# Optimization experiments

Measured on AMD Instinct MI355X. Metric: run time of the kernel, lower is better.

Reference implementation:

```python
import math
import jax, jax.numpy as jnp
import numpy as np

B, S, IN_DIM = 8, 1024, 3
D, H, FF, L, OUT = 512, 8, 2048, 4, 6
DH = D // H


def layernorm(x, g, b, eps=1e-5):
    mu = jnp.mean(x, axis=-1, keepdims=True)
    var = jnp.mean((x - mu) ** 2, axis=-1, keepdims=True)
    return (x - mu) * jax.lax.rsqrt(var + eps) * g + b


def positional_encoding(seq_len, d):
    pos = jnp.arange(seq_len, dtype=jnp.float32)[:, None]
    div = jnp.exp(jnp.arange(0, d, 2, dtype=jnp.float32) * (-math.log(10000.0) / d))
    pe = jnp.zeros((seq_len, d), dtype=jnp.float32)
    pe = pe.at[:, 0::2].set(jnp.sin(pos * div))
    pe = pe.at[:, 1::2].set(jnp.cos(pos * div))
    return pe  # [S, D]


def setup_inputs() -> dict:
    key = jax.random.key(0)
    ks = jax.random.split(key, 16)
    s = 0.02
    inp = {
        'x': jax.random.normal(ks[0], (B, S, IN_DIM), dtype=jnp.float32),
        'Wproj': jax.random.normal(ks[1], (IN_DIM, D), dtype=jnp.float32) * s,
        'bproj': jnp.zeros((D,), jnp.float32),
        'gp': jnp.ones((D,), jnp.float32), 'bp': jnp.zeros((D,), jnp.float32),
        'Wq': jax.random.normal(ks[2], (L, D, D), dtype=jnp.float32) * s,
        'Wk': jax.random.normal(ks[3], (L, D, D), dtype=jnp.float32) * s,
        'Wv': jax.random.normal(ks[4], (L, D, D), dtype=jnp.float32) * s,
        'Wo': jax.random.normal(ks[5], (L, D, D), dtype=jnp.float32) * s,
        'g1': jnp.ones((L, D), jnp.float32), 'b1': jnp.zeros((L, D), jnp.float32),
        'W1': jax.random.normal(ks[6], (L, D, FF), dtype=jnp.float32) * s,
        'W2': jax.random.normal(ks[7], (L, FF, D), dtype=jnp.float32) * s,
        'g2': jnp.ones((L, D), jnp.float32), 'b2': jnp.zeros((L, D), jnp.float32),
        'gf': jnp.ones((D,), jnp.float32), 'bf': jnp.zeros((D,), jnp.float32),
        'Wout': jax.random.normal(ks[8], (D, OUT), dtype=jnp.float32) * s,
        'bout': jnp.zeros((OUT,), jnp.float32),
    }
    return inp


def reference(x, Wproj, bproj, gp, bp, Wq, Wk, Wv, Wo, g1, b1,
              W1, W2, g2, b2, gf, bf, Wout, bout):
    # padding mask: True where all features are zero
    mask = jnp.sum(jnp.abs(x), axis=-1) == 0  # [B, S]
    h = x @ Wproj + bproj                     # [B, S, D]
    h = h + positional_encoding(h.shape[1], D)[None]
    h = layernorm(h, gp, bp)
    scale = 1.0 / math.sqrt(DH)
    for l in range(L):
        q = (h @ Wq[l]).reshape(B, S, H, DH)
        k = (h @ Wk[l]).reshape(B, S, H, DH)
        v = (h @ Wv[l]).reshape(B, S, H, DH)
        scores = jnp.einsum('bqhd,bkhd->bhqk', q, k) * scale  # [B,H,S,S]
        scores = jnp.where(mask[:, None, None, :], -jnp.inf, scores)
        attn = jax.nn.softmax(scores, axis=-1)
        o = jnp.einsum('bhqk,bkhd->bqhd', attn, v).reshape(B, S, D) @ Wo[l]
        h = layernorm(h + o, g1[l], b1[l])
        ff = jax.nn.silu(h @ W1[l]) @ W2[l]
        h = layernorm(h + ff, g2[l], b2[l])
    h = layernorm(h, gf, bf)
    not_pad = (~mask).astype(h.dtype)                      # [B, S]
    pooled = jnp.sum(h * not_pad[..., None], axis=1) / (
        jnp.sum(not_pad, axis=1, keepdims=True) + 1e-8)    # [B, D]
    return pooled @ Wout + bout                            # [B, OUT]
```

## Files before the change

### kernel.cpp

```cpp
#include <hip/hip_runtime.h>
#include <math.h>
#include <stdint.h>

namespace {

constexpr int Bc = 8, Sc = 1024, Dc = 512, Hc = 8, FFc = 2048, Lc = 4, OUTc = 6;
constexpr int QS = 1536;

typedef __attribute__((ext_vector_type(8))) short  bf16x8;
typedef __attribute__((ext_vector_type(4))) float  f32x4;

__device__ __forceinline__ void ld4(float d[4], const float* s) {
    float4 t = *(const float4*)s;
    d[0] = t.x; d[1] = t.y; d[2] = t.z; d[3] = t.w;
}
__device__ __forceinline__ float bf2f_s(short u) {
    union { uint32_t i; float f; } c; c.i = ((uint32_t)(unsigned short)u) << 16; return c.f;
}
__device__ __forceinline__ unsigned short f2bf(float f) {
    union { float f; uint32_t i; } c; c.f = f;
    uint32_t r = c.i + 0x7FFF + ((c.i >> 16) & 1);
    return (unsigned short)(r >> 16);
}
__device__ __forceinline__ unsigned short f2bf_fast(float f) {
    union { float f; uint32_t i; } c; c.f = f;
    return (unsigned short)((c.i + 0x8000u) >> 16);
}

#define GLDS16(gp, lp) __builtin_amdgcn_global_load_lds(                      \
    (const __attribute__((address_space(1))) uint32_t*)(gp),                  \
    (__attribute__((address_space(3))) uint32_t*)(lp), 16, 0, 0)

__global__ __launch_bounds__(256) void castAll(
    const float* __restrict__ Wq, const float* __restrict__ Wk,
    const float* __restrict__ Wv, const float* __restrict__ Wo,
    const float* __restrict__ W1, const float* __restrict__ W2,
    unsigned short* __restrict__ qkvT, unsigned short* __restrict__ WoT,
    unsigned short* __restrict__ W1T, unsigned short* __restrict__ W2T)
{
    const int t = blockIdx.x;
    const float* in; unsigned short* out; int K, N, k0, n0;
    if (t < 1024) {
        const int mat = t >> 6, l = mat >> 2, w = mat & 3;
        K = 512; N = 512;
        k0 = ((t >> 3) & 7) << 6; n0 = (t & 7) << 6;
        const float* ws4[4] = {Wq, Wk, Wv, Wo};
        in = ws4[w] + (size_t)l * 512 * 512;
        out = (w < 3) ? qkvT + (size_t)l * QS * 512 + (size_t)w * 512 * 512
                      : WoT + (size_t)l * 512 * 512;
    } else if (t < 2048) {
        const int u = t - 1024, l = u >> 8;
        K = 512; N = 2048;
        k0 = ((u >> 5) & 7) << 6; n0 = (u & 31) << 6;
        in = W1 + (size_t)l * 512 * 2048;
        out = W1T + (size_t)l * 2048 * 512;
    } else {
        const int u = t - 2048, l = u >> 8;
        K = 2048; N = 512;
        k0 = ((u >> 3) & 31) << 6; n0 = (u & 7) << 6;
        in = W2 + (size_t)l * 2048 * 512;
        out = W2T + (size_t)l * 512 * 2048;
    }
    __shared__ float tbuf[64][65];
    const int c = threadIdx.x & 63, r4 = threadIdx.x >> 6;
    #pragma unroll
    for (int it = 0; it < 16; ++it) {
        const int r = (it << 2) + r4;
        tbuf[r][c] = in[(size_t)(k0 + r) * N + n0 + c];
    }
    __syncthreads();
    #pragma unroll
    for (int it = 0; it < 16; ++it) {
        const int r = (it << 2) + r4;
        out[(size_t)(n0 + r) * K + k0 + c] = f2bf(tbuf[c][r]);
    }
}

__global__ __launch_bounds__(256) void proj_pe_ln(
    const float* __restrict__ x, const float* __restrict__ Wproj,
    const float* __restrict__ bproj, const float* __restrict__ gp,
    const float* __restrict__ bp, unsigned short* __restrict__ hbf,
    float* __restrict__ notpad, float* __restrict__ maskadd)
{
    const int wave = threadIdx.x >> 6, lane = threadIdx.x & 63;
    const int tok = (blockIdx.x << 2) + wave;
    const int s = tok & (Sc - 1);
    const float x0 = x[tok * 3 + 0], x1 = x[tok * 3 + 1], x2 = x[tok * 3 + 2];
    if (lane == 0) {
        const bool pad = (fabsf(x0) + fabsf(x1) + fabsf(x2) == 0.0f);
        notpad[tok]  = pad ? 0.0f : 1.0f;
        maskadd[tok] = pad ? -1e30f : 0.0f;
    }
    const float c = -logf(10000.0f) / (float)Dc;
    float v[8];
    float sum = 0.f, sumsq = 0.f;
    const int d0 = lane << 3;
    #pragma unroll
    for (int j = 0; j < 8; ++j) {
        const int d = d0 + j;
        float val = fmaf(x0, Wproj[d],
                    fmaf(x1, Wproj[Dc + d],
                    fmaf(x2, Wproj[2 * Dc + d], bproj[d])));
        const float arg = (float)s * expf((float)(d & ~1) * c);
        val += (d & 1) ? cosf(arg) : sinf(arg);
        v[j] = val;
        sum += val; sumsq += val * val;
    }
    #pragma unroll
    for (int m = 1; m < 64; m <<= 1) {
        sum   += __shfl_xor(sum, m, 64);
        sumsq += __shfl_xor(sumsq, m, 64);
    }
    const float mu = sum * (1.0f / Dc);
    const float rstd = rsqrtf(sumsq * (1.0f / Dc) - mu * mu + 1e-5f);
    float gg[8], bb[8];
    ld4(gg, gp + d0); ld4(gg + 4, gp + d0 + 4);
    ld4(bb, bp + d0); ld4(bb + 4, bp + d0 + 4);
    bf16x8 rb;
    #pragma unroll
    for (int j = 0; j < 8; ++j)
        rb[j] = (short)f2bf((v[j] - mu) * rstd * gg[j] + bb[j]);
    *(bf16x8*)(hbf + (size_t)tok * Dc + d0) = rb;
}

__global__ __launch_bounds__(256) void add_ln(
    const unsigned short* __restrict__ hin, const unsigned short* __restrict__ delta,
    const float* __restrict__ g, const float* __restrict__ b,
    unsigned short* __restrict__ hout)
{
    const int wave = threadIdx.x >> 6, lane = threadIdx.x & 63;
    const int tok = (blockIdx.x << 2) + wave;
    const int d0 = lane << 3;
    const size_t base = (size_t)tok * Dc + d0;
    const bf16x8 hv = *(const bf16x8*)(hin + base);
    const bf16x8 dv = *(const bf16x8*)(delta + base);
    float v[8];
    float sum = 0.f, sumsq = 0.f;
    #pragma unroll
    for (int j = 0; j < 8; ++j) {
        v[j] = bf2f_s(hv[j]) + bf2f_s(dv[j]);
        sum += v[j]; sumsq += v[j] * v[j];
    }
    #pragma unroll
    for (int m = 1; m < 64; m <<= 1) {
        sum   += __shfl_xor(sum, m, 64);
        sumsq += __shfl_xor(sumsq, m, 64);
    }
    const float mu = sum * (1.0f / Dc);
    const float rstd = rsqrtf(sumsq * (1.0f / Dc) - mu * mu + 1e-5f);
    float gg[8], bb[8];
    ld4(gg, g + d0); ld4(gg + 4, g + d0 + 4);
    ld4(bb, b + d0); ld4(bb + 4, b + d0 + 4);
    bf16x8 rb;
    #pragma unroll
    for (int j = 0; j < 8; ++j)
        rb[j] = (short)f2bf((v[j] - mu) * rstd * gg[j] + bb[j]);
    *(bf16x8*)(hout + base) = rb;
}

template<int EPI, int NT>
__global__ __launch_bounds__(256) void gemm_bf16(
    const unsigned short* __restrict__ A, const unsigned short* __restrict__ Bt,
    void* __restrict__ Cv, void* __restrict__ Cv2, int M, int N, int K)
{
    constexpr int JN = NT / 32;
    constexpr int TR = 140;
    constexpr int ABsz = 128 * 64 + NT * 64;
    constexpr int SMsz = (EPI == 3 && 128 * TR > ABsz) ? 128 * TR : ABsz;
    __shared__ unsigned short smem[SMsz];
    unsigned short* As = smem;
    unsigned short* Bs = smem + 128 * 64;
    const int tid = threadIdx.x;
    const int wave = tid >> 6, lane = tid & 63;
    const int m0 = blockIdx.y << 7;
    const int n0 = blockIdx.x * NT;
    const int wm = (wave >> 1) << 6;
    const int wn = (wave & 1) * (NT / 2);
    const int l15 = lane & 15;
    const int lg  = lane >> 4;
    const int grow  = lane >> 3;
    const int gcolk = ((lane & 7) ^ grow) << 3;

    f32x4 acc[4][JN] = {};

    for (int k0 = 0; k0 < K; k0 += 64) {
        __syncthreads();
        #pragma unroll
        for (int t = 0; t < 4; ++t) {
            const int rb = (t << 5) + (wave << 3);
            GLDS16(A + (size_t)(m0 + rb + grow) * K + k0 + gcolk, &As[rb * 64]);
        }
        #pragma unroll
        for (int t = 0; t < NT / 32; ++t) {
            const int rb = (t << 5) + (wave << 3);
            GLDS16(Bt + (size_t)(n0 + rb + grow) * K + k0 + gcolk, &Bs[rb * 64]);
        }
        __syncthreads();
        #pragma unroll
        for (int h = 0; h < 2; ++h) {
            const int sw = (((h << 2) + lg) ^ (l15 & 7)) << 3;
            bf16x8 af[4], bfr[JN];
            #pragma unroll
            for (int i = 0; i < 4; ++i)
                af[i] = *(const bf16x8*)&As[(wm + (i << 4) + l15) * 64 + sw];
            #pragma unroll
            for (int j = 0; j < JN; ++j)
                bfr[j] = *(const bf16x8*)&Bs[(wn + (j << 4) + l15) * 64 + sw];
            #pragma unroll
            for (int i = 0; i < 4; ++i)
                #pragma unroll
                for (int j = 0; j < JN; ++j)
                    acc[i][j] = __builtin_amdgcn_mfma_f32_16x16x32_bf16(
                        af[i], bfr[j], acc[i][j], 0, 0, 0);
        }
    }

    if constexpr (EPI == 3) {
        if (n0 >= 1024) {
            __syncthreads();
            unsigned short* Tr = smem;
            #pragma unroll
            for (int i = 0; i < 4; ++i)
                #pragma unroll
                for (int j = 0; j < JN; ++j)
                    #pragma unroll
                    for (int r = 0; r < 4; ++r)
                        Tr[(wn + (j << 4) + l15) * TR + wm + (i << 4) + (lg << 2) + r]
                            = f2bf(acc[i][j][r]);
            __syncthreads();
            const int bb = m0 >> 10, s0 = m0 & 1023;
            #pragma unroll
            for (int it = 0; it < 8; ++it) {
                const int idx = (it << 8) + tid;
                const int ln = idx >> 4, lmc = (idx & 15) << 3;
                const int gcol = n0 - 1024 + ln;
                const int head = gcol >> 6, dh = gcol & 63;
                *(bf16x8*)((unsigned short*)Cv2 +
                    (size_t)((((bb << 3) + head) << 6) + dh) * 1024 + s0 + lmc) =
                    *(const bf16x8*)&Tr[ln * TR + lmc];
            }
            return;
        }
    }

    const float qsc = 0.125f * 1.44269504f;
    const int crow0 = m0 + wm + (lg << 2);
    const int ccol0 = n0 + wn + l15;
    #pragma unroll
    for (int i = 0; i < 4; ++i)
        #pragma unroll
        for (int j = 0; j < JN; ++j)
            #pragma unroll
            for (int r = 0; r < 4; ++r) {
                const int row = crow0 + (i << 4) + r;
                const int col = ccol0 + (j << 4);
                float v = acc[i][j][r];
                if (EPI == 3) {
                    if (n0 < 512) v *= qsc;
                    ((unsigned short*)Cv)[(size_t)row * 1024 + col] = f2bf(v);
                } else {
                    if (EPI == 1) v = v / (1.0f + expf(-v));
                    ((unsigned short*)Cv)[(size_t)row * N + col] = f2bf(v);
                }
            }
}

__global__ __launch_bounds__(256) void attn_mfma(
    const unsigned short* __restrict__ qk,
    const unsigned short* __restrict__ vT,
    const float* __restrict__ maskadd,
    unsigned short* __restrict__ o)
{
    constexpr int PST = 132;
    __shared__ unsigned short Ks[2][128][32];
    __shared__ unsigned short Vs[4][64][32];
    __shared__ unsigned short Ps[4][16][PST];
    __shared__ float Madd[128];
    const int tid = threadIdx.x;
    const int wave = tid >> 6, lane = tid & 63;
    const int b  = blockIdx.x & 7;
    const int hh = (blockIdx.x >> 3) & 7;
    const int qt = blockIdx.x >> 6;
    const int q0 = qt << 7;
    const int l15 = lane & 15, lg = lane >> 4;
    const int srow = lane >> 2;
    const int scol = (lane & 3) << 3;

    #pragma unroll
    for (int t = 0; t < 2; ++t)
        #pragma unroll
        for (int p = 0; p < 2; ++p)
            GLDS16(qk + (size_t)((b << 10) + q0 + (t << 6) + (wave << 4) + srow) * 1024
                      + (hh << 6) + (p << 5) + scol,
                   &Ks[p][(t << 6) + (wave << 4)][0]);
    __syncthreads();
    bf16x8 qf[2][2];
    #pragma unroll
    for (int s = 0; s < 2; ++s)
        #pragma unroll
        for (int p = 0; p < 2; ++p)
            qf[s][p] = *(const bf16x8*)&Ks[p][(s << 6) + (wave << 4) + l15][lg << 3];

    f32x4 oacc[2][4] = {};
    float l_part[2][4] = {};

    for (int kt = 0; kt < 8; ++kt) {
        const int k0 = kt << 7;
        __syncthreads();
        #pragma unroll
        for (int t = 0; t < 2; ++t)
            #pragma unroll
            for (int p = 0; p < 2; ++p)
                GLDS16(qk + (size_t)((b << 10) + k0 + (t << 6) + (wave << 4) + srow) * 1024
                          + 512 + (hh << 6) + (p << 5) + scol,
                       &Ks[p][(t << 6) + (wave << 4)][0]);
        #pragma unroll
        for (int kp = 0; kp < 4; ++kp)
            GLDS16(vT + (size_t)((((b << 3) + hh) << 6) + (wave << 4) + srow) * 1024
                      + k0 + (kp << 5) + scol,
                   &Vs[kp][wave << 4][0]);
        if (tid < 128) Madd[tid] = maskadd[(b << 10) + k0 + tid];
        __syncthreads();

        f32x4 sacc[2][8] = {};
        #pragma unroll
        for (int j = 0; j < 8; ++j) {
            const bf16x8 kf0 = *(const bf16x8*)&Ks[0][(j << 4) + l15][lg << 3];
            const bf16x8 kf1 = *(const bf16x8*)&Ks[1][(j << 4) + l15][lg << 3];
            #pragma unroll
            for (int s = 0; s < 2; ++s) {
                sacc[s][j] = __builtin_amdgcn_mfma_f32_16x16x32_bf16(qf[s][0], kf0, sacc[s][j], 0, 0, 0);
                sacc[s][j] = __builtin_amdgcn_mfma_f32_16x16x32_bf16(qf[s][1], kf1, sacc[s][j], 0, 0, 0);
            }
        }

        bf16x8 vf[4][4];
        #pragma unroll
        for (int kp = 0; kp < 4; ++kp)
            #pragma unroll
            for (int j = 0; j < 4; ++j)
                vf[kp][j] = *(const bf16x8*)&Vs[kp][(j << 4) + l15][lg << 3];

        float ma[8];
        #pragma unroll
        for (int j = 0; j < 8; ++j) ma[j] = Madd[(j << 4) + l15];

        #pragma unroll
        for (int s = 0; s < 2; ++s) {
            #pragma unroll
            for (int j = 0; j < 8; ++j)
                #pragma unroll
                for (int r = 0; r < 4; ++r) {
                    const float p = exp2f(sacc[s][j][r] + ma[j]);
                    l_part[s][r] += p;
                    Ps[wave][(lg << 2) + r][(j << 4) + l15] = f2bf_fast(p);
                }
            __asm__ volatile("s_waitcnt lgkmcnt(0)" ::: "memory");
            #pragma unroll
            for (int kp = 0; kp < 4; ++kp) {
                const bf16x8 pa = *(const bf16x8*)&Ps[wave][l15][(kp << 5) + (lg << 3)];
                #pragma unroll
                for (int j = 0; j < 4; ++j)
                    oacc[s][j] = __builtin_amdgcn_mfma_f32_16x16x32_bf16(pa, vf[kp][j], oacc[s][j], 0, 0, 0);
            }
            __asm__ volatile("s_waitcnt lgkmcnt(0)" ::: "memory");
        }
    }

    #pragma unroll
    for (int s = 0; s < 2; ++s)
        #pragma unroll
        for (int r = 0; r < 4; ++r) {
            float l = l_part[s][r];
            #pragma unroll
            for (int m = 1; m < 16; m <<= 1) l += __shfl_xor(l, m, 64);
            l_part[s][r] = 1.0f / l;
        }
    #pragma unroll
    for (int s = 0; s < 2; ++s) {
        const int tokr = (b << 10) + q0 + (s << 6) + (wave << 4) + (lg << 2);
        #pragma unroll
        for (int j = 0; j < 4; ++j)
            #pragma unroll
            for (int r = 0; r < 4; ++r)
                o[(size_t)(tokr + r) * 512 + (hh << 6) + (j << 4) + l15] =
                    f2bf(oacc[s][j][r] * l_part[s][r]);
    }
}

__global__ __launch_bounds__(256) void pool_ln(
    const unsigned short* __restrict__ hbf, const float* __restrict__ notpad,
    const float* __restrict__ gf, const float* __restrict__ bfp,
    float* __restrict__ pooled, float* __restrict__ counts)
{
    __shared__ float sh[512];
    const int b = blockIdx.y, s0 = blockIdx.x << 5;
    const int wave = threadIdx.x >> 6, lane = threadIdx.x & 63;
    const int d0 = lane << 3;
    float gg[8], bb[8];
    ld4(gg, gf + d0); ld4(gg + 4, gf + d0 + 4);
    ld4(bb, bfp + d0); ld4(bb + 4, bfp + d0 + 4);
    float accv[8] = {};
    for (int t = 0; t < 8; ++t) {
        const int tok = (b << 10) + s0 + (wave << 3) + t;
        const float w = notpad[tok];
        const bf16x8 hv = *(const bf16x8*)(hbf + (size_t)tok * Dc + d0);
        float v[8], sum = 0.f, sumsq = 0.f;
        #pragma unroll
        for (int j = 0; j < 8; ++j) {
            v[j] = bf2f_s(hv[j]); sum += v[j]; sumsq += v[j] * v[j];
        }
        #pragma unroll
        for (int m = 1; m < 64; m <<= 1) {
            sum   += __shfl_xor(sum, m, 64);
            sumsq += __shfl_xor(sumsq, m, 64);
        }
        const float mu = sum * (1.0f / Dc);
        const float rstd = rsqrtf(sumsq * (1.0f / Dc) - mu * mu + 1e-5f);
        #pragma unroll
        for (int j = 0; j < 8; ++j)
            accv[j] = fmaf(w, (v[j] - mu) * rstd * gg[j] + bb[j], accv[j]);
    }
    sh[threadIdx.x] = 0.f; sh[threadIdx.x + 256] = 0.f;
    __syncthreads();
    #pragma unroll
    for (int j = 0; j < 8; ++j) atomicAdd(&sh[d0 + j], accv[j]);
    __syncthreads();
    atomicAdd(&pooled[b * Dc + threadIdx.x], sh[threadIdx.x]);
    atomicAdd(&pooled[b * Dc + 256 + threadIdx.x], sh[threadIdx.x + 256]);
    if (threadIdx.x < 32) {
        float w = notpad[(b << 10) + s0 + threadIdx.x];
        #pragma unroll
        for (int m = 1; m < 32; m <<= 1) w += __shfl_xor(w, m, 64);
        if (threadIdx.x == 0) atomicAdd(&counts[b], w);
    }
}

__global__ void out_kernel(
    const float* __restrict__ pooled, const float* __restrict__ counts,
    const float* __restrict__ Wout, const float* __restrict__ bout,
    float* __restrict__ out)
{
    const int bo = blockIdx.x;
    const int b = bo / OUTc, oc = bo % OUTc;
    const int lane = threadIdx.x;
    float acc = 0.f;
    for (int d = lane; d < Dc; d += 64)
        acc = fmaf(pooled[b * Dc + d], Wout[(size_t)d * OUTc + oc], acc);
    #pragma unroll
    for (int m = 1; m < 64; m <<= 1) acc += __shfl_xor(acc, m, 64);
    if (lane == 0) out[b * OUTc + oc] = acc / (counts[b] + 1e-8f) + bout[oc];
}

}

extern "C" void kernel_launch(void* const* d_in, const int* in_sizes, int n_in,
                              void* d_out, int out_size, void* d_ws, size_t ws_size,
                              hipStream_t stream)
{
    (void)in_sizes; (void)n_in; (void)out_size; (void)ws_size;
    const float* x     = (const float*)d_in[0];
    const float* Wproj = (const float*)d_in[1];
    const float* bproj = (const float*)d_in[2];
    const float* gp    = (const float*)d_in[3];
    const float* bp    = (const float*)d_in[4];
    const float* Wq    = (const float*)d_in[5];
    const float* Wk    = (const float*)d_in[6];
    const float* Wv    = (const float*)d_in[7];
    const float* Wo    = (const float*)d_in[8];
    const float* g1    = (const float*)d_in[9];
    const float* b1    = (const float*)d_in[10];
    const float* W1    = (const float*)d_in[11];
    const float* W2    = (const float*)d_in[12];
    const float* g2    = (const float*)d_in[13];
    const float* b2    = (const float*)d_in[14];
    const float* gf    = (const float*)d_in[15];
    const float* bf    = (const float*)d_in[16];
    const float* Wout  = (const float*)d_in[17];
    const float* bout  = (const float*)d_in[18];
    float* out = (float*)d_out;

    const size_t MiB = 1u << 20;
    char* base = (char*)d_ws;
    unsigned short* h_bf    = (unsigned short*)(base);
    unsigned short* qk_act  = (unsigned short*)(base + 24 * MiB);
    unsigned short* vT      = (unsigned short*)(base + 40 * MiB);
    unsigned short* ob_bf   = (unsigned short*)(base + 48 * MiB);
    unsigned short* bufB_bf = (unsigned short*)(base + 56 * MiB);
    unsigned short* ffa_bf  = (unsigned short*)(base + 24 * MiB);
    unsigned short* qkvT    = (unsigned short*)(base + 72 * MiB);
    unsigned short* WoT     = (unsigned short*)(base + 78 * MiB);
    unsigned short* W1T     = (unsigned short*)(base + 80 * MiB);
    unsigned short* W2T     = (unsigned short*)(base + 88 * MiB);
    float*          notpad  = (float*)(base + 96 * MiB);
    float*          maskadd = notpad + 8192;
    float*          pooled  = maskadd + 8192;
    float*          counts  = pooled + Bc * Dc;

    const int M = Bc * Sc;

    castAll<<<3072, 256, 0, stream>>>(Wq, Wk, Wv, Wo, W1, W2, qkvT, WoT, W1T, W2T);
    proj_pe_ln<<<M / 4, 256, 0, stream>>>(x, Wproj, bproj, gp, bp, h_bf, notpad, maskadd);

    for (int l = 0; l < Lc; ++l) {
        gemm_bf16<3, 128><<<dim3(QS / 128, M / 128), 256, 0, stream>>>(
            h_bf, qkvT + (size_t)l * QS * 512, qk_act, vT, M, QS, 512);
        attn_mfma<<<Bc * Hc * (Sc / 128), 256, 0, stream>>>(qk_act, vT, maskadd, ob_bf);
        gemm_bf16<2, 64><<<dim3(512 / 64, M / 128), 256, 0, stream>>>(
            ob_bf, WoT + (size_t)l * 512 * 512, bufB_bf, nullptr, M, 512, 512);
        add_ln<<<M / 4, 256, 0, stream>>>(h_bf, bufB_bf, g1 + (size_t)l * Dc, b1 + (size_t)l * Dc, h_bf);
        gemm_bf16<1, 128><<<dim3(FFc / 128, M / 128), 256, 0, stream>>>(
            h_bf, W1T + (size_t)l * FFc * 512, ffa_bf, nullptr, M, FFc, 512);
        gemm_bf16<2, 64><<<dim3(512 / 64, M / 128), 256, 0, stream>>>(
            ffa_bf, W2T + (size_t)l * 512 * FFc, bufB_bf, nullptr, M, 512, FFc);
        add_ln<<<M / 4, 256, 0, stream>>>(h_bf, bufB_bf, g2 + (size_t)l * Dc, b2 + (size_t)l * Dc, h_bf);
    }

    hipMemsetAsync(pooled, 0, (size_t)(Bc * Dc + Bc) * sizeof(float), stream);
    pool_ln<<<dim3(Sc / 32, Bc), 256, 0, stream>>>(h_bf, notpad, gf, bf, pooled, counts);
    out_kernel<<<Bc * OUTc, 64, 0, stream>>>(pooled, counts, Wout, bout, out);
}
```

Baseline: 824.1 us.

## Fold LayerNorm into GEMMs via weight folding and epilogue partial stats

Removes the standalone add+LayerNorm kernels. Gamma and beta are folded into the QKV and W1 weights at cast time, along with correction vectors, so the following GEMM epilogue applies the normalization from per-row mean and rstd. The Wo and W2 GEMM epilogues now do the residual add on the un-normalized stream and write per-row partial sum and sum-of-squares, which the next kernel reduces. This saves two full activation read/write passes per layer, at the cost of heavier epilogues, atomics in the weight cast, and different bf16 rounding points.

```diff
diff --git a/kernel.cpp b/kernel.cpp
--- a/kernel.cpp
+++ b/kernel.cpp
@@ -13,6 +13,9 @@
 __device__ __forceinline__ void ld4(float d[4], const float* s) {
     float4 t = *(const float4*)s;
     d[0] = t.x; d[1] = t.y; d[2] = t.z; d[3] = t.w;
+}
+__device__ __forceinline__ float bf2f_u(unsigned short u) {
+    union { uint32_t i; float f; } c; c.i = ((uint32_t)u) << 16; return c.f;
 }
 __device__ __forceinline__ float bf2f_s(short u) {
     union { uint32_t i; float f; } c; c.i = ((uint32_t)(unsigned short)u) << 16; return c.f;
@@ -35,25 +38,44 @@
     const float* __restrict__ Wq, const float* __restrict__ Wk,
     const float* __restrict__ Wv, const float* __restrict__ Wo,
     const float* __restrict__ W1, const float* __restrict__ W2,
+    const float* __restrict__ gp, const float* __restrict__ bp,
+    const float* __restrict__ g1, const float* __restrict__ b1,
+    const float* __restrict__ g2, const float* __restrict__ b2,
     unsigned short* __restrict__ qkvT, unsigned short* __restrict__ WoT,
-    unsigned short* __restrict__ W1T, unsigned short* __restrict__ W2T)
+    unsigned short* __restrict__ W1T, unsigned short* __restrict__ W2T,
+    float* __restrict__ c1qkv, float* __restrict__ c2qkv,
+    float* __restrict__ c1w1, float* __restrict__ c2w1)
 {
     const int t = blockIdx.x;
     const float* in; unsigned short* out; int K, N, k0, n0;
+    bool fold = false;
+    const float *gamma = nullptr, *beta = nullptr;
+    float *cv1 = nullptr, *cv2 = nullptr;
     if (t < 1024) {
         const int mat = t >> 6, l = mat >> 2, w = mat & 3;
         K = 512; N = 512;
         k0 = ((t >> 3) & 7) << 6; n0 = (t & 7) << 6;
         const float* ws4[4] = {Wq, Wk, Wv, Wo};
         in = ws4[w] + (size_t)l * 512 * 512;
-        out = (w < 3) ? qkvT + (size_t)l * QS * 512 + (size_t)w * 512 * 512
-                      : WoT + (size_t)l * 512 * 512;
+        if (w < 3) {
+            out = qkvT + (size_t)l * QS * 512 + (size_t)w * 512 * 512;
+            fold = true;
+            gamma = (l == 0) ? gp : g2 + (size_t)(l - 1) * 512;
+            beta  = (l == 0) ? bp : b2 + (size_t)(l - 1) * 512;
+            cv1 = c1qkv + (size_t)l * QS + w * 512;
+            cv2 = c2qkv + (size_t)l * QS + w * 512;
+        } else {
+            out = WoT + (size_t)l * 512 * 512;
+        }
     } else if (t < 2048) {
         const int u = t - 1024, l = u >> 8;
         K = 512; N = 2048;
         k0 = ((u >> 5) & 7) << 6; n0 = (u & 31) << 6;
         in = W1 + (size_t)l * 512 * 2048;
         out = W1T + (size_t)l * 2048 * 512;
+        fold = true;
+        gamma = g1 + (size_t)l * 512; beta = b1 + (size_t)l * 512;
+        cv1 = c1w1 + (size_t)l * 2048; cv2 = c2w1 + (size_t)l * 2048;
     } else {
         const int u = t - 2048, l = u >> 8;
         K = 2048; N = 512;
@@ -62,7 +84,12 @@
         out = W2T + (size_t)l * 512 * 2048;
     }
     __shared__ float tbuf[64][65];
+    __shared__ float gls[64], bls[64];
     const int c = threadIdx.x & 63, r4 = threadIdx.x >> 6;
+    if (fold && threadIdx.x < 64) {
+        gls[threadIdx.x] = gamma[k0 + threadIdx.x];
+        bls[threadIdx.x] = beta[k0 + threadIdx.x];
+    }
     #pragma unroll
     for (int it = 0; it < 16; ++it) {
         const int r = (it << 2) + r4;
@@ -72,15 +99,28 @@
     #pragma unroll
     for (int it = 0; it < 16; ++it) {
         const int r = (it << 2) + r4;
-        out[(size_t)(n0 + r) * K + k0 + c] = f2bf(tbuf[c][r]);
-    }
-}
-
-__global__ __launch_bounds__(256) void proj_pe_ln(
+        float v = tbuf[c][r];
+        if (fold) v *= gls[c];
+        out[(size_t)(n0 + r) * K + k0 + c] = f2bf(v);
+    }
+    if (fold && threadIdx.x < 64) {
+        float a1 = 0.f, a2 = 0.f;
+        #pragma unroll
+        for (int cc = 0; cc < 64; ++cc) {
+            const float w = tbuf[cc][threadIdx.x];
+            a1 = fmaf(gls[cc], w, a1);
+            a2 = fmaf(bls[cc], w, a2);
+        }
+        atomicAdd(cv1 + n0 + threadIdx.x, a1);
+        atomicAdd(cv2 + n0 + threadIdx.x, a2);
+    }
+}
+
+__global__ __launch_bounds__(256) void proj_pe(
     const float* __restrict__ x, const float* __restrict__ Wproj,
-    const float* __restrict__ bproj, const float* __restrict__ gp,
-    const float* __restrict__ bp, unsigned short* __restrict__ hbf,
-    float* __restrict__ notpad, float* __restrict__ maskadd)
+    const float* __restrict__ bproj, unsigned short* __restrict__ res,
+    float* __restrict__ stats, float* __restrict__ notpad,
+    float* __restrict__ maskadd)
 {
     const int wave = threadIdx.x >> 6, lane = threadIdx.x & 63;
     const int tok = (blockIdx.x << 2) + wave;
@@ -92,9 +132,9 @@
         maskadd[tok] = pad ? -1e30f : 0.0f;
     }
     const float c = -logf(10000.0f) / (float)Dc;
-    float v[8];
+    const int d0 = lane << 3;
     float sum = 0.f, sumsq = 0.f;
-    const int d0 = lane << 3;
+    bf16x8 rb;
     #pragma unroll
     for (int j = 0; j < 8; ++j) {
         const int d = d0 + j;
@@ -103,71 +143,38 @@
                     fmaf(x2, Wproj[2 * Dc + d], bproj[d])));
         const float arg = (float)s * expf((float)(d & ~1) * c);
         val += (d & 1) ? cosf(arg) : sinf(arg);
-        v[j] = val;
-        sum += val; sumsq += val * val;
-    }
+        rb[j] = (short)f2bf(val);
+        const float rv = bf2f_s(rb[j]);
+        sum += rv; sumsq += rv * rv;
+    }
+    *(bf16x8*)(res + (size_t)tok * Dc + d0) = rb;
     #pragma unroll
     for (int m = 1; m < 64; m <<= 1) {
         sum   += __shfl_xor(sum, m, 64);
         sumsq += __shfl_xor(sumsq, m, 64);
     }
-    const float mu = sum * (1.0f / Dc);
-    const float rstd = rsqrtf(sumsq * (1.0f / Dc) - mu * mu + 1e-5f);
-    float gg[8], bb[8];
-    ld4(gg, gp + d0); ld4(gg + 4, gp + d0 + 4);
-    ld4(bb, bp + d0); ld4(bb + 4, bp + d0 + 4);
-    bf16x8 rb;
-    #pragma unroll
-    for (int j = 0; j < 8; ++j)
-        rb[j] = (short)f2bf((v[j] - mu) * rstd * gg[j] + bb[j]);
-    *(bf16x8*)(hbf + (size_t)tok * Dc + d0) = rb;
-}
-
-__global__ __launch_bounds__(256) void add_ln(
-    const unsigned short* __restrict__ hin, const unsigned short* __restrict__ delta,
-    const float* __restrict__ g, const float* __restrict__ b,
-    unsigned short* __restrict__ hout)
-{
-    const int wave = threadIdx.x >> 6, lane = threadIdx.x & 63;
-    const int tok = (blockIdx.x << 2) + wave;
-    const int d0 = lane << 3;
-    const size_t base = (size_t)tok * Dc + d0;
-    const bf16x8 hv = *(const bf16x8*)(hin + base);
-    const bf16x8 dv = *(const bf16x8*)(delta + base);
-    float v[8];
-    float sum = 0.f, sumsq = 0.f;
-    #pragma unroll
-    for (int j = 0; j < 8; ++j) {
-        v[j] = bf2f_s(hv[j]) + bf2f_s(dv[j]);
-        sum += v[j]; sumsq += v[j] * v[j];
-    }
-    #pragma unroll
-    for (int m = 1; m < 64; m <<= 1) {
-        sum   += __shfl_xor(sum, m, 64);
-        sumsq += __shfl_xor(sumsq, m, 64);
-    }
-    const float mu = sum * (1.0f / Dc);
-    const float rstd = rsqrtf(sumsq * (1.0f / Dc) - mu * mu + 1e-5f);
-    float gg[8], bb[8];
-    ld4(gg, g + d0); ld4(gg + 4, g + d0 + 4);
-    ld4(bb, b + d0); ld4(bb + 4, b + d0 + 4);
-    bf16x8 rb;
-    #pragma unroll
-    for (int j = 0; j < 8; ++j)
-        rb[j] = (short)f2bf((v[j] - mu) * rstd * gg[j] + bb[j]);
-    *(bf16x8*)(hout + base) = rb;
+    if (lane == 0) {
+        stats[(size_t)tok * 32 + 0] = sum;
+        stats[(size_t)tok * 32 + 1] = sumsq;
+    }
 }
 
 template<int EPI, int NT>
 __global__ __launch_bounds__(256) void gemm_bf16(
     const unsigned short* __restrict__ A, const unsigned short* __restrict__ Bt,
-    void* __restrict__ Cv, void* __restrict__ Cv2, int M, int N, int K)
+    void* __restrict__ Cv, void* __restrict__ Cv2,
+    const float* __restrict__ statsIn, int npart,
+    const float* __restrict__ c1, const float* __restrict__ c2,
+    const unsigned short* __restrict__ resIn,
+    const float* __restrict__ gcol, const float* __restrict__ bcol,
+    float* __restrict__ partOut, int M, int N, int K)
 {
     constexpr int JN = NT / 32;
     constexpr int TR = 140;
     constexpr int ABsz = 128 * 64 + NT * 64;
     constexpr int SMsz = (EPI == 3 && 128 * TR > ABsz) ? 128 * TR : ABsz;
     __shared__ unsigned short smem[SMsz];
+    __shared__ float muS[128], rsS[128];
     unsigned short* As = smem;
     unsigned short* Bs = smem + 128 * 64;
     const int tid = threadIdx.x;
@@ -215,61 +222,114 @@
         }
     }
 
-    if constexpr (EPI == 3) {
-        if (n0 >= 1024) {
-            __syncthreads();
-            unsigned short* Tr = smem;
-            #pragma unroll
-            for (int i = 0; i < 4; ++i)
-                #pragma unroll
-                for (int j = 0; j < JN; ++j)
+    __syncthreads();
+    if (tid < 128) {
+        float s1 = 0.f, s2 = 0.f;
+        const float* pr = statsIn + (size_t)(m0 + tid) * 32;
+        for (int p = 0; p < npart; ++p) { s1 += pr[2 * p]; s2 += pr[2 * p + 1]; }
+        const float mu = s1 * (1.0f / 512.0f);
+        muS[tid] = mu;
+        rsS[tid] = rsqrtf(s2 * (1.0f / 512.0f) - mu * mu + 1e-5f);
+    }
+    __syncthreads();
+
+    if constexpr (EPI == 3 || EPI == 1) {
+        float c1v[JN], c2v[JN];
+        const int ccol0 = n0 + wn + l15;
+        #pragma unroll
+        for (int j = 0; j < JN; ++j) {
+            c1v[j] = c1[ccol0 + (j << 4)];
+            c2v[j] = c2[ccol0 + (j << 4)];
+        }
+        if constexpr (EPI == 3) {
+            if (n0 >= 1024) {
+                unsigned short* Tr = smem;
+                #pragma unroll
+                for (int i = 0; i < 4; ++i)
                     #pragma unroll
-                    for (int r = 0; r < 4; ++r)
-                        Tr[(wn + (j << 4) + l15) * TR + wm + (i << 4) + (lg << 2) + r]
-                            = f2bf(acc[i][j][r]);
-            __syncthreads();
-            const int bb = m0 >> 10, s0 = m0 & 1023;
-            #pragma unroll
-            for (int it = 0; it < 8; ++it) {
-                const int idx = (it << 8) + tid;
-                const int ln = idx >> 4, lmc = (idx & 15) << 3;
-                const int gcol = n0 - 1024 + ln;
-                const int head = gcol >> 6, dh = gcol & 63;
-                *(bf16x8*)((unsigned short*)Cv2 +
-                    (size_t)((((bb << 3) + head) << 6) + dh) * 1024 + s0 + lmc) =
-                    *(const bf16x8*)&Tr[ln * TR + lmc];
+                    for (int j = 0; j < JN; ++j)
+                        #pragma unroll
+                        for (int r = 0; r < 4; ++r) {
+                            const int lr = wm + (i << 4) + (lg << 2) + r;
+                            const float v = rsS[lr] * (acc[i][j][r] - muS[lr] * c1v[j]) + c2v[j];
+                            Tr[(wn + (j << 4) + l15) * TR + lr] = f2bf(v);
+                        }
+                __syncthreads();
+                const int bb = m0 >> 10, s0 = m0 & 1023;
+                #pragma unroll
+                for (int it = 0; it < 8; ++it) {
+                    const int idx = (it << 8) + tid;
+                    const int ln = idx >> 4, lmc = (idx & 15) << 3;
+                    const int gcol2 = n0 - 1024 + ln;
+                    const int head = gcol2 >> 6, dh = gcol2 & 63;
+                    *(bf16x8*)((unsigned short*)Cv2 +
+                        (size_t)((((bb << 3) + head) << 6) + dh) * 1024 + s0 + lmc) =
+                        *(const bf16x8*)&smem[ln * TR + lmc];
+                }
+                return;
             }
-            return;
-        }
-    }
-
-    const float qsc = 0.125f * 1.44269504f;
-    const int crow0 = m0 + wm + (lg << 2);
-    const int ccol0 = n0 + wn + l15;
-    #pragma unroll
-    for (int i = 0; i < 4; ++i)
-        #pragma unroll
-        for (int j = 0; j < JN; ++j)
+        }
+        const float qsc = 0.125f * 1.44269504f;
+        #pragma unroll
+        for (int i = 0; i < 4; ++i)
+            #pragma unroll
+            for (int j = 0; j < JN; ++j)
+                #pragma unroll
+                for (int r = 0; r < 4; ++r) {
+                    const int lr = wm + (i << 4) + (lg << 2) + r;
+                    const int row = m0 + lr;
+                    const int col = ccol0 + (j << 4);
+                    float v = rsS[lr] * (acc[i][j][r] - muS[lr] * c1v[j]) + c2v[j];
+                    if (EPI == 3) {
+                        if (n0 < 512) v *= qsc;
+                        ((unsigned short*)Cv)[(size_t)row * 1024 + col] = f2bf(v);
+                    } else {
+                        v = v / (1.0f + expf(-v));
+                        ((unsigned short*)Cv)[(size_t)row * N + col] = f2bf(v);
+                    }
+                }
+    } else {
+        float gv[JN], bv[JN];
+        const int ccol0 = n0 + wn + l15;
+        #pragma unroll
+        for (int j = 0; j < JN; ++j) {
+            gv[j] = gcol[ccol0 + (j << 4)];
+            bv[j] = bcol[ccol0 + (j << 4)];
+        }
+        const int slot = (blockIdx.x << 1) | (wave & 1);
+        #pragma unroll
+        for (int i = 0; i < 4; ++i)
             #pragma unroll
             for (int r = 0; r < 4; ++r) {
-                const int row = crow0 + (i << 4) + r;
-                const int col = ccol0 + (j << 4);
-                float v = acc[i][j][r];
-                if (EPI == 3) {
-                    if (n0 < 512) v *= qsc;
-                    ((unsigned short*)Cv)[(size_t)row * 1024 + col] = f2bf(v);
-                } else {
-                    if (EPI == 1) v = v / (1.0f + expf(-v));
-                    ((unsigned short*)Cv)[(size_t)row * N + col] = f2bf(v);
+                const int lr = wm + (i << 4) + (lg << 2) + r;
+                const int row = m0 + lr;
+                float s1 = 0.f, s2 = 0.f;
+                #pragma unroll
+                for (int j = 0; j < JN; ++j) {
+                    const int col = ccol0 + (j << 4);
+                    const float hp = bf2f_u(resIn[(size_t)row * 512 + col]);
+                    const float hn = (hp - muS[lr]) * rsS[lr] * gv[j] + bv[j];
+                    const unsigned short rb = f2bf(hn + acc[i][j][r]);
+                    ((unsigned short*)Cv)[(size_t)row * 512 + col] = rb;
+                    const float rv = bf2f_u(rb);
+                    s1 += rv; s2 += rv * rv;
+                }
+                #pragma unroll
+                for (int m = 1; m < 16; m <<= 1) {
+                    s1 += __shfl_xor(s1, m, 64);
+                    s2 += __shfl_xor(s2, m, 64);
+                }
+                if (l15 == 0) {
+                    partOut[(size_t)row * 32 + slot * 2 + 0] = s1;
+                    partOut[(size_t)row * 32 + slot * 2 + 1] = s2;
                 }
             }
+    }
 }
 
 __global__ __launch_bounds__(256) void attn_mfma(
-    const unsigned short* __restrict__ qk,
-    const unsigned short* __restrict__ vT,
-    const float* __restrict__ maskadd,
-    unsigned short* __restrict__ o)
+    const unsigned short* __restrict__ qk, const unsigned short* __restrict__ vT,
+    const float* __restrict__ maskadd, unsigned short* __restrict__ o)
 {
     constexpr int PST = 132;
     __shared__ unsigned short Ks[2][128][32];
@@ -389,7 +449,9 @@
 }
 
 __global__ __launch_bounds__(256) void pool_ln(
-    const unsigned short* __restrict__ hbf, const float* __restrict__ notpad,
+    const unsigned short* __restrict__ res, const float* __restrict__ stats,
+    const float* __restrict__ notpad,
+    const float* __restrict__ g2l, const float* __restrict__ b2l,
     const float* __restrict__ gf, const float* __restrict__ bfp,
     float* __restrict__ pooled, float* __restrict__ counts)
 {
@@ -397,18 +459,30 @@
     const int b = blockIdx.y, s0 = blockIdx.x << 5;
     const int wave = threadIdx.x >> 6, lane = threadIdx.x & 63;
     const int d0 = lane << 3;
-    float gg[8], bb[8];
+    float g2v[8], b2v[8], gg[8], bb[8];
+    ld4(g2v, g2l + d0); ld4(g2v + 4, g2l + d0 + 4);
+    ld4(b2v, b2l + d0); ld4(b2v + 4, b2l + d0 + 4);
     ld4(gg, gf + d0); ld4(gg + 4, gf + d0 + 4);
     ld4(bb, bfp + d0); ld4(bb + 4, bfp + d0 + 4);
     float accv[8] = {};
     for (int t = 0; t < 8; ++t) {
         const int tok = (b << 10) + s0 + (wave << 3) + t;
         const float w = notpad[tok];
-        const bf16x8 hv = *(const bf16x8*)(hbf + (size_t)tok * Dc + d0);
-        float v[8], sum = 0.f, sumsq = 0.f;
+        float s1 = stats[(size_t)tok * 32 + ((lane & 15) << 1)];
+        float s2 = stats[(size_t)tok * 32 + ((lane & 15) << 1) + 1];
+        #pragma unroll
+        for (int m = 1; m < 16; m <<= 1) {
+            s1 += __shfl_xor(s1, m, 64);
+            s2 += __shfl_xor(s2, m, 64);
+        }
+        const float mu2 = s1 * (1.0f / Dc);
+        const float rs2 = rsqrtf(s2 * (1.0f / Dc) - mu2 * mu2 + 1e-5f);
+        const bf16x8 hv = *(const bf16x8*)(res + (size_t)tok * Dc + d0);
+        float h2[8], sum = 0.f, sumsq = 0.f;
         #pragma unroll
         for (int j = 0; j < 8; ++j) {
-            v[j] = bf2f_s(hv[j]); sum += v[j]; sumsq += v[j] * v[j];
+            h2[j] = (bf2f_s(hv[j]) - mu2) * rs2 * g2v[j] + b2v[j];
+            sum += h2[j]; sumsq += h2[j] * h2[j];
         }
         #pragma unroll
         for (int m = 1; m < 64; m <<= 1) {
@@ -419,7 +493,7 @@
         const float rstd = rsqrtf(sumsq * (1.0f / Dc) - mu * mu + 1e-5f);
         #pragma unroll
         for (int j = 0; j < 8; ++j)
-            accv[j] = fmaf(w, (v[j] - mu) * rstd * gg[j] + bb[j], accv[j]);
+            accv[j] = fmaf(w, (h2[j] - mu) * rstd * gg[j] + bb[j], accv[j]);
     }
     sh[threadIdx.x] = 0.f; sh[threadIdx.x + 256] = 0.f;
     __syncthreads();
@@ -482,41 +556,59 @@
 
     const size_t MiB = 1u << 20;
     char* base = (char*)d_ws;
-    unsigned short* h_bf    = (unsigned short*)(base);
+    unsigned short* res     = (unsigned short*)(base);
+    unsigned short* res1    = (unsigned short*)(base + 8 * MiB);
+    float*          partA   = (float*)(base + 16 * MiB);
+    float*          partB   = (float*)(base + 17 * MiB);
+    float*          cvec    = (float*)(base + 18 * MiB);
+    float*          c1qkv   = cvec;
+    float*          c2qkv   = cvec + 6144;
+    float*          c1w1    = cvec + 12288;
+    float*          c2w1    = cvec + 20480;
+    float*          pooled  = cvec + 28672;
+    float*          counts  = cvec + 32768;
+    float*          notpad  = (float*)(base + 19 * MiB);
+    float*          maskadd = notpad + 8192;
     unsigned short* qk_act  = (unsigned short*)(base + 24 * MiB);
     unsigned short* vT      = (unsigned short*)(base + 40 * MiB);
     unsigned short* ob_bf   = (unsigned short*)(base + 48 * MiB);
-    unsigned short* bufB_bf = (unsigned short*)(base + 56 * MiB);
     unsigned short* ffa_bf  = (unsigned short*)(base + 24 * MiB);
     unsigned short* qkvT    = (unsigned short*)(base + 72 * MiB);
     unsigned short* WoT     = (unsigned short*)(base + 78 * MiB);
     unsigned short* W1T     = (unsigned short*)(base + 80 * MiB);
     unsigned short* W2T     = (unsigned short*)(base + 88 * MiB);
-    float*          notpad  = (float*)(base + 96 * MiB);
-    float*          maskadd = notpad + 8192;
-    float*          pooled  = maskadd + 8192;
-    float*          counts  = pooled + Bc * Dc;
 
     const int M = Bc * Sc;
 
-    castAll<<<3072, 256, 0, stream>>>(Wq, Wk, Wv, Wo, W1, W2, qkvT, WoT, W1T, W2T);
-    proj_pe_ln<<<M / 4, 256, 0, stream>>>(x, Wproj, bproj, gp, bp, h_bf, notpad, maskadd);
+    hipMemsetAsync(cvec, 0, (size_t)(32768 + 8) * sizeof(float), stream);
+    castAll<<<3072, 256, 0, stream>>>(Wq, Wk, Wv, Wo, W1, W2,
+        gp, bp, g1, b1, g2, b2, qkvT, WoT, W1T, W2T, c1qkv, c2qkv, c1w1, c2w1);
+    proj_pe<<<M / 4, 256, 0, stream>>>(x, Wproj, bproj, res, partA, notpad, maskadd);
 
     for (int l = 0; l < Lc; ++l) {
+        const int np = (l == 0) ? 1 : 16;
+        const float* gprev = (l == 0) ? gp : g2 + (size_t)(l - 1) * 512;
+        const float* bprev = (l == 0) ? bp : b2 + (size_t)(l - 1) * 512;
         gemm_bf16<3, 128><<<dim3(QS / 128, M / 128), 256, 0, stream>>>(
-            h_bf, qkvT + (size_t)l * QS * 512, qk_act, vT, M, QS, 512);
+            res, qkvT + (size_t)l * QS * 512, qk_act, vT,
+            partA, np, c1qkv + (size_t)l * QS, c2qkv + (size_t)l * QS,
+            nullptr, nullptr, nullptr, nullptr, M, QS, 512);
         attn_mfma<<<Bc * Hc * (Sc / 128), 256, 0, stream>>>(qk_act, vT, maskadd, ob_bf);
-        gemm_bf16<2, 64><<<dim3(512 / 64, M / 128), 256, 0, stream>>>(
-            ob_bf, WoT + (size_t)l * 512 * 512, bufB_bf, nullptr, M, 512, 512);
-        add_ln<<<M / 4, 256, 0, stream>>>(h_bf, bufB_bf, g1 + (size_t)l * Dc, b1 + (size_t)l * Dc, h_bf);
+        gemm_bf16<4, 64><<<dim3(512 / 64, M / 128), 256, 0, stream>>>(
+            ob_bf, WoT + (size_t)l * 512 * 512, res1, nullptr,
+            partA, np, nullptr, nullptr, res, gprev, bprev, partB, M, 512, 512);
         gemm_bf16<1, 128><<<dim3(FFc / 128, M / 128), 256, 0, stream>>>(
-            h_bf, W1T + (size_t)l * FFc * 512, ffa_bf, nullptr, M, FFc, 512);
-        gemm_bf16<2, 64><<<dim3(512 / 64, M / 128), 256, 0, stream>>>(
-            ffa_bf, W2T + (size_t)l * 512 * FFc, bufB_bf, nullptr, M, 512, FFc);
-        add_ln<<<M / 4, 256, 0, stream>>>(h_bf, bufB_bf, g2 + (size_t)l * Dc, b2 + (size_t)l * Dc, h_bf);
-    }
-
-    hipMemsetAsync(pooled, 0, (size_t)(Bc * Dc + Bc) * sizeof(float), stream);
-    pool_ln<<<dim3(Sc / 32, Bc), 256, 0, stream>>>(h_bf, notpad, gf, bf, pooled, counts);
+            res1, W1T + (size_t)l * FFc * 512, ffa_bf, nullptr,
+            partB, 16, c1w1 + (size_t)l * FFc, c2w1 + (size_t)l * FFc,
+            nullptr, nullptr, nullptr, nullptr, M, FFc, 512);
+        gemm_bf16<5, 64><<<dim3(512 / 64, M / 128), 256, 0, stream>>>(
+            ffa_bf, W2T + (size_t)l * 512 * FFc, res, nullptr,
+            partB, 16, nullptr, nullptr, res1,
+            g1 + (size_t)l * 512, b1 + (size_t)l * 512, partA, M, 512, FFc);
+    }
+
+    pool_ln<<<dim3(Sc / 32, Bc), 256, 0, stream>>>(
+        res, partA, notpad, g2 + (size_t)3 * 512, b2 + (size_t)3 * 512,
+        gf, bf, pooled, counts);
     out_kernel<<<Bc * OUTc, 64, 0, stream>>>(pooled, counts, Wout, bout, out);
 }
```

Measured after the change: 926.1 us. 1.12x slower.
